# Kernel optimization log

Measured on AMD Instinct MI355X. Metric: run time of the kernel, lower is better.

The kernel has to match this reference:

```python
import jax, jax.numpy as jnp
import numpy as np

EPS = 1e-12  # matches torch F.normalize default eps


def _l2norm(x):
    n = jnp.linalg.norm(x, axis=-1, keepdims=True)
    return x / jnp.maximum(n, EPS)


def setup_inputs() -> dict:
    key = jax.random.key(0)
    k1, k2, k3, k4 = jax.random.split(key, 4)
    B, N, Lq, Ld, D = 64, 16, 32, 256, 128
    query_rep = jax.random.normal(k1, (B, Lq, D), jnp.float32)
    doc_reps = jax.random.normal(k2, (B, N, Ld, D), jnp.float32)
    doc_mask = jax.random.randint(k3, (B, N, Ld), 0, 2).astype(jnp.int32)
    labels = jax.random.normal(k4, (B, 2 * N), jnp.float32)
    return {"query_rep": query_rep, "doc_reps": doc_reps,
            "doc_mask": doc_mask, "labels": labels}


def reference(query_rep, doc_reps, doc_mask, labels):
    # ColBERT MaxSim: normalize query tokens (no mask, as in original),
    # mask+normalize doc tokens, bmm, max over doc tokens, sum over query tokens.
    q = _l2norm(query_rep)                                   # [B,Lq,D]
    d = _l2norm(doc_reps * doc_mask[..., None].astype(doc_reps.dtype))  # [B,N,Ld,D]
    tok = jnp.einsum('bqd,bnld->bnql', q, d)                 # [B,N,Lq,Ld]
    scores = tok.max(axis=-1).sum(axis=-1)                   # [B,N]

    # Pairwise ranking loss
    N = scores.shape[1]
    ys = labels[:, :N]
    idx = labels[:, N:]
    diffs = jnp.triu(scores[:, :, None] - scores[:, None, :])    # [B,N,N], lower tri zeroed
    weights = jnp.abs(idx[:, :, None] - idx[:, None, :])
    pairs = (ys[:, :, None] - ys[:, None, :]) > 0
    losses = jnp.log1p(jnp.exp(-diffs)) * weights
    return jnp.sum(jnp.where(pairs, losses, 0.0))
```

## Files before the change

### kernel.cpp

```cpp
#include <hip/hip_runtime.h>
#include <cmath>

#define EPSN 1e-12f

typedef _Float16 half8 __attribute__((ext_vector_type(8)));
typedef float f32x4 __attribute__((ext_vector_type(4)));

__global__ __launch_bounds__(256, 4) void scores_kernel(
    const float* __restrict__ qr, const float* __restrict__ doc,
    const int* __restrict__ mask, float* __restrict__ pmax) {
    __shared__ __align__(16) char Aimg[16384];
    __shared__ __align__(16) char Bimg[16384];
    __shared__ float ssPart[256];
    __shared__ float invS[128];
    __shared__ float wq[4][32];

    int t = threadIdx.x, g = blockIdx.x;
    int bn = g >> 1, h = g & 1, b = g >> 5;
    int w = t >> 6, lane = t & 63, col = lane & 15;
    int tok = t & 127, kh = t >> 7;

    const float4* dsrc = (const float4*)(doc + ((size_t)bn * 256 + h * 128 + tok) * 128) + kh * 4;
    float4 rA0 = dsrc[0], rA1 = dsrc[1], rA2 = dsrc[2], rA3 = dsrc[3];
    float4 rB0, rB1, rB2, rB3;
    int mymask = 0;
    if (t < 128) mymask = mask[bn * 256 + h * 128 + t];

    {
        int row = t >> 3, jb = t & 7;
        const float4* qsrc = (const float4*)(qr + ((size_t)b * 32 + row) * 128 + jb * 16);
        float4 v[4];
#pragma unroll
        for (int i = 0; i < 4; ++i) v[i] = qsrc[i];
        float ss = 0.f;
#pragma unroll
        for (int i = 0; i < 4; ++i)
            ss += v[i].x*v[i].x + v[i].y*v[i].y + v[i].z*v[i].z + v[i].w*v[i].w;
        ss += __shfl_xor(ss, 1); ss += __shfl_xor(ss, 2); ss += __shfl_xor(ss, 4);
        float inv = 1.0f / fmaxf(sqrtf(ss), EPSN);
        int qt = row >> 4, kstep = jb >> 1;
#pragma unroll
        for (int khh = 0; khh < 2; ++khh) {
            float xs[8] = { v[2*khh].x,   v[2*khh].y,   v[2*khh].z,   v[2*khh].w,
                            v[2*khh+1].x, v[2*khh+1].y, v[2*khh+1].z, v[2*khh+1].w };
            half8 hh, hl;
#pragma unroll
            for (int e = 0; e < 8; ++e) {
                float x = xs[e] * inv;
                _Float16 hv = (_Float16)x;
                hh[e] = hv;
                hl[e] = (_Float16)(x - (float)hv);
            }
            int quad = (jb & 1) * 2 + khh;
            int base = ((qt * 4 + kstep) * 2) * 1024 + ((row & 15) + quad * 16) * 16;
            *(half8*)(Aimg + base)        = hh;
            *(half8*)(Aimg + base + 1024) = hl;
        }
    }
    asm volatile("s_waitcnt lgkmcnt(0)" ::: "memory");
    __builtin_amdgcn_s_barrier();

    f32x4 acc[2][2];
    f32x4 zero = {0.f, 0.f, 0.f, 0.f};
    acc[0][0] = zero; acc[0][1] = zero; acc[1][0] = zero; acc[1][1] = zero;
    float ss_d = 0.f;

    int tile8 = tok >> 4;
    int bo_base = tile8 * 2048 + (2 * kh) * 256 + (tok & 15) * 16;

#define CHUNK(C, P0, P1, P2, P3, N0, N1, N2, N3, ISLAST) do {                 \
    if (!(ISLAST)) {                                                          \
        N0 = dsrc[(C + 1) * 8 + 0]; N1 = dsrc[(C + 1) * 8 + 1];               \
        N2 = dsrc[(C + 1) * 8 + 2]; N3 = dsrc[(C + 1) * 8 + 3];               \
    }                                                                         \
    ss_d += P0.x*P0.x + P0.y*P0.y + P0.z*P0.z + P0.w*P0.w;                    \
    ss_d += P1.x*P1.x + P1.y*P1.y + P1.z*P1.z + P1.w*P1.w;                    \
    ss_d += P2.x*P2.x + P2.y*P2.y + P2.z*P2.z + P2.w*P2.w;                    \
    ss_d += P3.x*P3.x + P3.y*P3.y + P3.z*P3.z + P3.w*P3.w;                    \
    {                                                                         \
        float xa[8] = { P0.x, P0.y, P0.z, P0.w, P1.x, P1.y, P1.z, P1.w };     \
        float xb[8] = { P2.x, P2.y, P2.z, P2.w, P3.x, P3.y, P3.z, P3.w };     \
        half8 hha, hla, hhb, hlb;                                             \
        _Pragma("unroll")                                                     \
        for (int e = 0; e < 8; ++e) {                                         \
            float x = xa[e]; _Float16 hv = (_Float16)x;                       \
            hha[e] = hv; hla[e] = (_Float16)(x - (float)hv);                  \
            float y = xb[e]; _Float16 hw = (_Float16)y;                       \
            hhb[e] = hw; hlb[e] = (_Float16)(y - (float)hw);                  \
        }                                                                     \
        *(half8*)(Bimg + bo_base)              = hha;                         \
        *(half8*)(Bimg + bo_base + 1024)       = hla;                         \
        *(half8*)(Bimg + bo_base + 256)        = hhb;                         \
        *(half8*)(Bimg + bo_base + 256 + 1024) = hlb;                         \
    }                                                                         \
    if (ISLAST) ssPart[t] = ss_d;                                             \
    asm volatile("s_waitcnt lgkmcnt(0)" ::: "memory");                        \
    __builtin_amdgcn_s_barrier();                                             \
    if ((ISLAST) && t < 128) {                                                \
        float sst = ssPart[t] + ssPart[t + 128];                              \
        invS[t] = mymask ? (1.0f / fmaxf(sqrtf(sst), EPSN)) : 0.0f;           \
    }                                                                         \
    {                                                                         \
        int lo = lane << 4;                                                   \
        half8 a0h = *(const half8*)(Aimg + (((C) * 2 + 0) << 10) + lo);       \
        half8 a0l = *(const half8*)(Aimg + (((C) * 2 + 1) << 10) + lo);       \
        half8 a1h = *(const half8*)(Aimg + (((4 + (C)) * 2 + 0) << 10) + lo); \
        half8 a1l = *(const half8*)(Aimg + (((4 + (C)) * 2 + 1) << 10) + lo); \
        _Pragma("unroll")                                                     \
        for (int nt = 0; nt < 2; ++nt) {                                      \
            int tile = w * 2 + nt;                                            \
            half8 bh = *(const half8*)(Bimg + tile * 2048 + lo);              \
            half8 bl = *(const half8*)(Bimg + tile * 2048 + 1024 + lo);       \
            acc[0][nt] = __builtin_amdgcn_mfma_f32_16x16x32_f16(a0l, bh, acc[0][nt], 0, 0, 0); \
            acc[0][nt] = __builtin_amdgcn_mfma_f32_16x16x32_f16(a0h, bl, acc[0][nt], 0, 0, 0); \
            acc[0][nt] = __builtin_amdgcn_mfma_f32_16x16x32_f16(a0h, bh, acc[0][nt], 0, 0, 0); \
            acc[1][nt] = __builtin_amdgcn_mfma_f32_16x16x32_f16(a1l, bh, acc[1][nt], 0, 0, 0); \
            acc[1][nt] = __builtin_amdgcn_mfma_f32_16x16x32_f16(a1h, bl, acc[1][nt], 0, 0, 0); \
            acc[1][nt] = __builtin_amdgcn_mfma_f32_16x16x32_f16(a1h, bh, acc[1][nt], 0, 0, 0); \
        }                                                                     \
    }                                                                         \
    asm volatile("s_waitcnt lgkmcnt(0)" ::: "memory");                        \
    __builtin_amdgcn_s_barrier();                                             \
} while (0)

    CHUNK(0, rA0, rA1, rA2, rA3, rB0, rB1, rB2, rB3, false);
    CHUNK(1, rB0, rB1, rB2, rB3, rA0, rA1, rA2, rA3, false);
    CHUNK(2, rA0, rA1, rA2, rA3, rB0, rB1, rB2, rB3, false);
    CHUNK(3, rB0, rB1, rB2, rB3, rA0, rA1, rA2, rA3, true);
#undef CHUNK

    float inv0 = invS[w * 32 + col];
    float inv1 = invS[w * 32 + 16 + col];
    float m8[8];
#pragma unroll
    for (int qt = 0; qt < 2; ++qt)
#pragma unroll
        for (int rr = 0; rr < 4; ++rr)
            m8[qt * 4 + rr] = fmaxf(acc[qt][0][rr] * inv0, acc[qt][1][rr] * inv1);
#pragma unroll
    for (int off = 1; off < 16; off <<= 1)
#pragma unroll
        for (int i = 0; i < 8; ++i) m8[i] = fmaxf(m8[i], __shfl_xor(m8[i], off));
    if (col == 0) {
        int rg = lane >> 4;
#pragma unroll
        for (int qt = 0; qt < 2; ++qt)
#pragma unroll
            for (int rr = 0; rr < 4; ++rr) wq[w][qt * 16 + rg * 4 + rr] = m8[qt * 4 + rr];
    }
    __syncthreads();
    if (w == 0 && lane < 32) {
        float v = fmaxf(fmaxf(wq[0][lane], wq[1][lane]), fmaxf(wq[2][lane], wq[3][lane]));
        pmax[(size_t)g * 32 + lane] = v;
    }
}

__global__ __launch_bounds__(256) void lossb_kernel(const float* __restrict__ pmax,
                                                    const float* __restrict__ labels,
                                                    float* __restrict__ partial) {
    __shared__ float pmL[1024];
    __shared__ float sc[16], ysS[16], idxS[16];
    __shared__ float wsum[4];
    int b = blockIdx.x, t = threadIdx.x;
    ((float4*)pmL)[t] = ((const float4*)(pmax + (size_t)b * 1024))[t];
    if (t < 16) { ysS[t] = labels[b * 32 + t]; idxS[t] = labels[b * 32 + 16 + t]; }
    __syncthreads();
    {
        int n = t >> 4, qq = t & 15;
        float v = fmaxf(pmL[n * 64 + qq],      pmL[n * 64 + 32 + qq])
                + fmaxf(pmL[n * 64 + 16 + qq], pmL[n * 64 + 48 + qq]);
        v += __shfl_xor(v, 1); v += __shfl_xor(v, 2);
        v += __shfl_xor(v, 4); v += __shfl_xor(v, 8);
        if (qq == 0) sc[n] = v;
    }
    __syncthreads();
    int i = t >> 4, j = t & 15;
    float v = 0.f;
    if (ysS[i] - ysS[j] > 0.f) {
        float wgt = fabsf(idxS[i] - idxS[j]);
        float d = (i <= j) ? (sc[i] - sc[j]) : 0.f;
        v = log1pf(expf(-d)) * wgt;
    }
#pragma unroll
    for (int off = 1; off < 64; off <<= 1) v += __shfl_xor(v, off);
    int lane = t & 63;
    if (lane == 0) wsum[t >> 6] = v;
    __syncthreads();
    if (t == 0) partial[b] = wsum[0] + wsum[1] + wsum[2] + wsum[3];
}

__global__ void lossfin_kernel(const float* __restrict__ partial, float* __restrict__ out) {
    int t = threadIdx.x;
    float v = partial[t];
#pragma unroll
    for (int off = 1; off < 64; off <<= 1) v += __shfl_xor(v, off);
    if (t == 0) out[0] = v;
}

extern "C" void kernel_launch(void* const* d_in, const int* in_sizes, int n_in,
                              void* d_out, int out_size, void* d_ws, size_t ws_size,
                              hipStream_t stream) {
    const float* qr     = (const float*)d_in[0];
    const float* doc    = (const float*)d_in[1];
    const int*   dmask  = (const int*)d_in[2];
    const float* labels = (const float*)d_in[3];
    float* out = (float*)d_out;

    float* pmax    = (float*)d_ws;
    float* partial = pmax + 2048 * 32;

    scores_kernel<<<2048, 256, 0, stream>>>(qr, doc, dmask, pmax);
    lossb_kernel<<<64, 256, 0, stream>>>(pmax, labels, partial);
    lossfin_kernel<<<1, 64, 0, stream>>>(partial, out);
}
```

Before: 35.01 us.

## Coalesce doc loads, use shuffle norm reduction, and merge loss kernels

```diff
diff --git a/kernel.cpp b/kernel.cpp
--- a/kernel.cpp
+++ b/kernel.cpp
@@ -4,6 +4,7 @@
 #define EPSN 1e-12f
 
 typedef _Float16 half8 __attribute__((ext_vector_type(8)));
+typedef _Float16 half4 __attribute__((ext_vector_type(4)));
 typedef float f32x4 __attribute__((ext_vector_type(4)));
 
 __global__ __launch_bounds__(256, 4) void scores_kernel(
@@ -11,20 +12,25 @@
     const int* __restrict__ mask, float* __restrict__ pmax) {
     __shared__ __align__(16) char Aimg[16384];
     __shared__ __align__(16) char Bimg[16384];
-    __shared__ float ssPart[256];
     __shared__ float invS[128];
+    __shared__ int   maskS[128];
     __shared__ float wq[4][32];
 
     int t = threadIdx.x, g = blockIdx.x;
     int bn = g >> 1, h = g & 1, b = g >> 5;
     int w = t >> 6, lane = t & 63, col = lane & 15;
-    int tok = t & 127, kh = t >> 7;
-
-    const float4* dsrc = (const float4*)(doc + ((size_t)bn * 256 + h * 128 + tok) * 128) + kh * 4;
-    float4 rA0 = dsrc[0], rA1 = dsrc[1], rA2 = dsrc[2], rA3 = dsrc[3];
+
+    int u  = t >> 3;
+    int kq = t & 7;
+
+    const float4* dbase = (const float4*)(doc + ((size_t)bn * 256 + h * 128) * 128);
+    int fi0 = u * 32 + kq;
+
+    float4 rA0 = dbase[fi0 + 0], rA1 = dbase[fi0 + 1024];
+    float4 rA2 = dbase[fi0 + 2048], rA3 = dbase[fi0 + 3072];
     float4 rB0, rB1, rB2, rB3;
-    int mymask = 0;
-    if (t < 128) mymask = mask[bn * 256 + h * 128 + t];
+
+    if (t < 128) maskS[t] = mask[bn * 256 + h * 128 + t];
 
     {
         int row = t >> 3, jb = t & 7;
@@ -63,42 +69,53 @@
     f32x4 acc[2][2];
     f32x4 zero = {0.f, 0.f, 0.f, 0.f};
     acc[0][0] = zero; acc[0][1] = zero; acc[1][0] = zero; acc[1][1] = zero;
-    float ss_d = 0.f;
-
-    int tile8 = tok >> 4;
-    int bo_base = tile8 * 2048 + (2 * kh) * 256 + (tok & 15) * 16;
+    float ss0 = 0.f, ss1 = 0.f, ss2 = 0.f, ss3 = 0.f;
+
+    int bwbase = (u >> 4) * 2048 + (((kq >> 1) * 16 + (u & 15)) << 4) + (kq & 1) * 8;
+
+#define CVT4(P, HH, HL) do {                                                  \
+    float xs_[4] = { P.x, P.y, P.z, P.w };                                    \
+    _Pragma("unroll")                                                         \
+    for (int e_ = 0; e_ < 4; ++e_) {                                          \
+        float x_ = xs_[e_]; _Float16 hv_ = (_Float16)x_;                      \
+        HH[e_] = hv_; HL[e_] = (_Float16)(x_ - (float)hv_);                   \
+    }                                                                         \
+} while (0)
 
 #define CHUNK(C, P0, P1, P2, P3, N0, N1, N2, N3, ISLAST) do {                 \
     if (!(ISLAST)) {                                                          \
-        N0 = dsrc[(C + 1) * 8 + 0]; N1 = dsrc[(C + 1) * 8 + 1];               \
-        N2 = dsrc[(C + 1) * 8 + 2]; N3 = dsrc[(C + 1) * 8 + 3];               \
-    }                                                                         \
-    ss_d += P0.x*P0.x + P0.y*P0.y + P0.z*P0.z + P0.w*P0.w;                    \
-    ss_d += P1.x*P1.x + P1.y*P1.y + P1.z*P1.z + P1.w*P1.w;                    \
-    ss_d += P2.x*P2.x + P2.y*P2.y + P2.z*P2.z + P2.w*P2.w;                    \
-    ss_d += P3.x*P3.x + P3.y*P3.y + P3.z*P3.z + P3.w*P3.w;                    \
+        N0 = dbase[fi0 + (C + 1) * 8];        N1 = dbase[fi0 + 1024 + (C + 1) * 8]; \
+        N2 = dbase[fi0 + 2048 + (C + 1) * 8]; N3 = dbase[fi0 + 3072 + (C + 1) * 8]; \
+    }                                                                         \
+    ss0 += P0.x*P0.x + P0.y*P0.y + P0.z*P0.z + P0.w*P0.w;                     \
+    ss1 += P1.x*P1.x + P1.y*P1.y + P1.z*P1.z + P1.w*P1.w;                     \
+    ss2 += P2.x*P2.x + P2.y*P2.y + P2.z*P2.z + P2.w*P2.w;                     \
+    ss3 += P3.x*P3.x + P3.y*P3.y + P3.z*P3.z + P3.w*P3.w;                     \
     {                                                                         \
-        float xa[8] = { P0.x, P0.y, P0.z, P0.w, P1.x, P1.y, P1.z, P1.w };     \
-        float xb[8] = { P2.x, P2.y, P2.z, P2.w, P3.x, P3.y, P3.z, P3.w };     \
-        half8 hha, hla, hhb, hlb;                                             \
-        _Pragma("unroll")                                                     \
-        for (int e = 0; e < 8; ++e) {                                         \
-            float x = xa[e]; _Float16 hv = (_Float16)x;                       \
-            hha[e] = hv; hla[e] = (_Float16)(x - (float)hv);                  \
-            float y = xb[e]; _Float16 hw = (_Float16)y;                       \
-            hhb[e] = hw; hlb[e] = (_Float16)(y - (float)hw);                  \
-        }                                                                     \
-        *(half8*)(Bimg + bo_base)              = hha;                         \
-        *(half8*)(Bimg + bo_base + 1024)       = hla;                         \
-        *(half8*)(Bimg + bo_base + 256)        = hhb;                         \
-        *(half8*)(Bimg + bo_base + 256 + 1024) = hlb;                         \
-    }                                                                         \
-    if (ISLAST) ssPart[t] = ss_d;                                             \
+        half4 h0, l0, h1, l1, h2, l2, h3, l3;                                 \
+        CVT4(P0, h0, l0); CVT4(P1, h1, l1); CVT4(P2, h2, l2); CVT4(P3, h3, l3); \
+        *(half4*)(Bimg + bwbase + 0)            = h0;                         \
+        *(half4*)(Bimg + bwbase + 1024)         = l0;                         \
+        *(half4*)(Bimg + bwbase + 4096)         = h1;                         \
+        *(half4*)(Bimg + bwbase + 4096 + 1024)  = l1;                         \
+        *(half4*)(Bimg + bwbase + 8192)         = h2;                         \
+        *(half4*)(Bimg + bwbase + 8192 + 1024)  = l2;                         \
+        *(half4*)(Bimg + bwbase + 12288)        = h3;                         \
+        *(half4*)(Bimg + bwbase + 12288 + 1024) = l3;                         \
+    }                                                                         \
     asm volatile("s_waitcnt lgkmcnt(0)" ::: "memory");                        \
     __builtin_amdgcn_s_barrier();                                             \
-    if ((ISLAST) && t < 128) {                                                \
-        float sst = ssPart[t] + ssPart[t + 128];                              \
-        invS[t] = mymask ? (1.0f / fmaxf(sqrtf(sst), EPSN)) : 0.0f;           \
+    if (ISLAST) {                                                             \
+        ss0 += __shfl_xor(ss0, 1); ss0 += __shfl_xor(ss0, 2); ss0 += __shfl_xor(ss0, 4); \
+        ss1 += __shfl_xor(ss1, 1); ss1 += __shfl_xor(ss1, 2); ss1 += __shfl_xor(ss1, 4); \
+        ss2 += __shfl_xor(ss2, 1); ss2 += __shfl_xor(ss2, 2); ss2 += __shfl_xor(ss2, 4); \
+        ss3 += __shfl_xor(ss3, 1); ss3 += __shfl_xor(ss3, 2); ss3 += __shfl_xor(ss3, 4); \
+        if (kq == 0) {                                                        \
+            invS[u]      = maskS[u]      ? (1.0f / fmaxf(sqrtf(ss0), EPSN)) : 0.0f; \
+            invS[u + 32] = maskS[u + 32] ? (1.0f / fmaxf(sqrtf(ss1), EPSN)) : 0.0f; \
+            invS[u + 64] = maskS[u + 64] ? (1.0f / fmaxf(sqrtf(ss2), EPSN)) : 0.0f; \
+            invS[u + 96] = maskS[u + 96] ? (1.0f / fmaxf(sqrtf(ss3), EPSN)) : 0.0f; \
+        }                                                                     \
     }                                                                         \
     {                                                                         \
         int lo = lane << 4;                                                   \
@@ -128,6 +145,7 @@
     CHUNK(2, rA0, rA1, rA2, rA3, rB0, rB1, rB2, rB3, false);
     CHUNK(3, rB0, rB1, rB2, rB3, rA0, rA1, rA2, rA3, true);
 #undef CHUNK
+#undef CVT4
 
     float inv0 = invS[w * 32 + col];
     float inv1 = invS[w * 32 + 16 + col];
@@ -155,46 +173,50 @@
     }
 }
 
-__global__ __launch_bounds__(256) void lossb_kernel(const float* __restrict__ pmax,
+__global__ __launch_bounds__(1024) void loss_kernel(const float* __restrict__ pmax,
                                                     const float* __restrict__ labels,
-                                                    float* __restrict__ partial) {
-    __shared__ float pmL[1024];
-    __shared__ float sc[16], ysS[16], idxS[16];
-    __shared__ float wsum[4];
-    int b = blockIdx.x, t = threadIdx.x;
-    ((float4*)pmL)[t] = ((const float4*)(pmax + (size_t)b * 1024))[t];
-    if (t < 16) { ysS[t] = labels[b * 32 + t]; idxS[t] = labels[b * 32 + 16 + t]; }
+                                                    float* __restrict__ out) {
+    __shared__ float scL[1024];
+    __shared__ float labL[2048];
+    __shared__ float wsum[16];
+    int t = threadIdx.x;
+    labL[t] = labels[t];
+    labL[t + 1024] = labels[t + 1024];
+    {
+        const float4* p0 = (const float4*)(pmax + (size_t)t * 64);
+        float s = 0.f;
+#pragma unroll
+        for (int i = 0; i < 8; ++i) {
+            float4 a = p0[i];
+            float4 bq = p0[i + 8];
+            s += fmaxf(a.x, bq.x) + fmaxf(a.y, bq.y) + fmaxf(a.z, bq.z) + fmaxf(a.w, bq.w);
+        }
+        scL[t] = s;
+    }
     __syncthreads();
-    {
-        int n = t >> 4, qq = t & 15;
-        float v = fmaxf(pmL[n * 64 + qq],      pmL[n * 64 + 32 + qq])
-                + fmaxf(pmL[n * 64 + 16 + qq], pmL[n * 64 + 48 + qq]);
-        v += __shfl_xor(v, 1); v += __shfl_xor(v, 2);
-        v += __shfl_xor(v, 4); v += __shfl_xor(v, 8);
-        if (qq == 0) sc[n] = v;
-    }
+    float total = 0.f;
+#pragma unroll
+    for (int it = 0; it < 16; ++it) {
+        int p = t + it * 1024;
+        int b = p >> 8, ij = p & 255, i = ij >> 4, j = ij & 15;
+        float ysi = labL[b * 32 + i], ysj = labL[b * 32 + j];
+        if (ysi - ysj > 0.f) {
+            float wgt = fabsf(labL[b * 32 + 16 + i] - labL[b * 32 + 16 + j]);
+            float d = (i <= j) ? (scL[b * 16 + i] - scL[b * 16 + j]) : 0.f;
+            total += log1pf(expf(-d)) * wgt;
+        }
+    }
+#pragma unroll
+    for (int off = 1; off < 64; off <<= 1) total += __shfl_xor(total, off);
+    int lane = t & 63;
+    if (lane == 0) wsum[t >> 6] = total;
     __syncthreads();
-    int i = t >> 4, j = t & 15;
-    float v = 0.f;
-    if (ysS[i] - ysS[j] > 0.f) {
-        float wgt = fabsf(idxS[i] - idxS[j]);
-        float d = (i <= j) ? (sc[i] - sc[j]) : 0.f;
-        v = log1pf(expf(-d)) * wgt;
-    }
-#pragma unroll
-    for (int off = 1; off < 64; off <<= 1) v += __shfl_xor(v, off);
-    int lane = t & 63;
-    if (lane == 0) wsum[t >> 6] = v;
-    __syncthreads();
-    if (t == 0) partial[b] = wsum[0] + wsum[1] + wsum[2] + wsum[3];
-}
-
-__global__ void lossfin_kernel(const float* __restrict__ partial, float* __restrict__ out) {
-    int t = threadIdx.x;
-    float v = partial[t];
-#pragma unroll
-    for (int off = 1; off < 64; off <<= 1) v += __shfl_xor(v, off);
-    if (t == 0) out[0] = v;
+    if (t < 64) {
+        float v = (t < 16) ? wsum[t] : 0.f;
+#pragma unroll
+        for (int off = 1; off < 64; off <<= 1) v += __shfl_xor(v, off);
+        if (t == 0) out[0] = v;
+    }
 }
 
 extern "C" void kernel_launch(void* const* d_in, const int* in_sizes, int n_in,
@@ -206,10 +228,8 @@
     const float* labels = (const float*)d_in[3];
     float* out = (float*)d_out;
 
-    float* pmax    = (float*)d_ws;
-    float* partial = pmax + 2048 * 32;
+    float* pmax = (float*)d_ws;
 
     scores_kernel<<<2048, 256, 0, stream>>>(qr, doc, dmask, pmax);
-    lossb_kernel<<<64, 256, 0, stream>>>(pmax, labels, partial);
-    lossfin_kernel<<<1, 64, 0, stream>>>(partial, out);
+    loss_kernel<<<1, 1024, 0, stream>>>(pmax, labels, out);
 }
```

New measurement: 55.91 us. 59.7% more time.

## Process full document per block and merge loss into single kernel

Applied to the files above, without the earlier changes.

```diff
diff --git a/kernel.cpp b/kernel.cpp
--- a/kernel.cpp
+++ b/kernel.cpp
@@ -8,23 +8,23 @@
 
 __global__ __launch_bounds__(256, 4) void scores_kernel(
     const float* __restrict__ qr, const float* __restrict__ doc,
-    const int* __restrict__ mask, float* __restrict__ pmax) {
+    const int* __restrict__ mask, float* __restrict__ scores) {
     __shared__ __align__(16) char Aimg[16384];
     __shared__ __align__(16) char Bimg[16384];
     __shared__ float ssPart[256];
     __shared__ float invS[128];
+    __shared__ int   maskS[256];
     __shared__ float wq[4][32];
 
     int t = threadIdx.x, g = blockIdx.x;
-    int bn = g >> 1, h = g & 1, b = g >> 5;
+    int b = g >> 4;
     int w = t >> 6, lane = t & 63, col = lane & 15;
     int tok = t & 127, kh = t >> 7;
 
-    const float4* dsrc = (const float4*)(doc + ((size_t)bn * 256 + h * 128 + tok) * 128) + kh * 4;
+    const float4* dsrc = (const float4*)(doc + ((size_t)g * 256 + tok) * 128) + kh * 4;
     float4 rA0 = dsrc[0], rA1 = dsrc[1], rA2 = dsrc[2], rA3 = dsrc[3];
     float4 rB0, rB1, rB2, rB3;
-    int mymask = 0;
-    if (t < 128) mymask = mask[bn * 256 + h * 128 + t];
+    maskS[t] = mask[g * 256 + t];
 
     {
         int row = t >> 3, jb = t & 7;
@@ -68,10 +68,10 @@
     int tile8 = tok >> 4;
     int bo_base = tile8 * 2048 + (2 * kh) * 256 + (tok & 15) * 16;
 
-#define CHUNK(C, P0, P1, P2, P3, N0, N1, N2, N3, ISLAST) do {                 \
-    if (!(ISLAST)) {                                                          \
-        N0 = dsrc[(C + 1) * 8 + 0]; N1 = dsrc[(C + 1) * 8 + 1];               \
-        N2 = dsrc[(C + 1) * 8 + 2]; N3 = dsrc[(C + 1) * 8 + 3];               \
+#define CHUNK(H, C, P0, P1, P2, P3, N0, N1, N2, N3, PREF, NEXTOFF, LASTC) do { \
+    if (PREF) {                                                               \
+        N0 = dsrc[(NEXTOFF) + 0]; N1 = dsrc[(NEXTOFF) + 1];                   \
+        N2 = dsrc[(NEXTOFF) + 2]; N3 = dsrc[(NEXTOFF) + 3];                   \
     }                                                                         \
     ss_d += P0.x*P0.x + P0.y*P0.y + P0.z*P0.z + P0.w*P0.w;                    \
     ss_d += P1.x*P1.x + P1.y*P1.y + P1.z*P1.z + P1.w*P1.w;                    \
@@ -93,12 +93,12 @@
         *(half8*)(Bimg + bo_base + 256)        = hhb;                         \
         *(half8*)(Bimg + bo_base + 256 + 1024) = hlb;                         \
     }                                                                         \
-    if (ISLAST) ssPart[t] = ss_d;                                             \
+    if (LASTC) { ssPart[t] = ss_d; ss_d = 0.f; }                              \
     asm volatile("s_waitcnt lgkmcnt(0)" ::: "memory");                        \
     __builtin_amdgcn_s_barrier();                                             \
-    if ((ISLAST) && t < 128) {                                                \
+    if ((LASTC) && t < 128) {                                                 \
         float sst = ssPart[t] + ssPart[t + 128];                              \
-        invS[t] = mymask ? (1.0f / fmaxf(sqrtf(sst), EPSN)) : 0.0f;           \
+        invS[t] = maskS[((H) << 7) | t] ? (1.0f / fmaxf(sqrtf(sst), EPSN)) : 0.0f; \
     }                                                                         \
     {                                                                         \
         int lo = lane << 4;                                                   \
@@ -123,78 +123,92 @@
     __builtin_amdgcn_s_barrier();                                             \
 } while (0)
 
-    CHUNK(0, rA0, rA1, rA2, rA3, rB0, rB1, rB2, rB3, false);
-    CHUNK(1, rB0, rB1, rB2, rB3, rA0, rA1, rA2, rA3, false);
-    CHUNK(2, rA0, rA1, rA2, rA3, rB0, rB1, rB2, rB3, false);
-    CHUNK(3, rB0, rB1, rB2, rB3, rA0, rA1, rA2, rA3, true);
+#define EPI_TILE(FIRST) do {                                                  \
+    float inv0 = invS[w * 32 + col];                                          \
+    float inv1 = invS[w * 32 + 16 + col];                                     \
+    float m8[8];                                                              \
+    _Pragma("unroll")                                                         \
+    for (int qt = 0; qt < 2; ++qt)                                            \
+        _Pragma("unroll")                                                     \
+        for (int rr = 0; rr < 4; ++rr)                                        \
+            m8[qt * 4 + rr] = fmaxf(acc[qt][0][rr] * inv0, acc[qt][1][rr] * inv1); \
+    _Pragma("unroll")                                                         \
+    for (int off = 1; off < 16; off <<= 1)                                    \
+        _Pragma("unroll")                                                     \
+        for (int i = 0; i < 8; ++i) m8[i] = fmaxf(m8[i], __shfl_xor(m8[i], off)); \
+    if (col == 0) {                                                           \
+        int rg = lane >> 4;           \
+        _Pragma("unroll")                                                     \
+        for (int qt = 0; qt < 2; ++qt)                                        \
+            _Pragma("unroll")                                                 \
+            for (int rr = 0; rr < 4; ++rr) {                                  \
+                int idx = qt * 16 + rg * 4 + rr;                              \
+                wq[w][idx] = (FIRST) ? m8[qt * 4 + rr]                        \
+                                     : fmaxf(wq[w][idx], m8[qt * 4 + rr]);    \
+            }                                                                 \
+    }                                                                         \
+} while (0)
+
+    CHUNK(0, 0, rA0, rA1, rA2, rA3, rB0, rB1, rB2, rB3, 1, 8,    0);
+    CHUNK(0, 1, rB0, rB1, rB2, rB3, rA0, rA1, rA2, rA3, 1, 16,   0);
+    CHUNK(0, 2, rA0, rA1, rA2, rA3, rB0, rB1, rB2, rB3, 1, 24,   0);
+    CHUNK(0, 3, rB0, rB1, rB2, rB3, rA0, rA1, rA2, rA3, 1, 4096, 1);
+    EPI_TILE(true);
+    acc[0][0] = zero; acc[0][1] = zero; acc[1][0] = zero; acc[1][1] = zero;
+    CHUNK(1, 0, rA0, rA1, rA2, rA3, rB0, rB1, rB2, rB3, 1, 4104, 0);
+    CHUNK(1, 1, rB0, rB1, rB2, rB3, rA0, rA1, rA2, rA3, 1, 4112, 0);
+    CHUNK(1, 2, rA0, rA1, rA2, rA3, rB0, rB1, rB2, rB3, 1, 4120, 0);
+    CHUNK(1, 3, rB0, rB1, rB2, rB3, rA0, rA1, rA2, rA3, 0, 0,    1);
+    EPI_TILE(false);
 #undef CHUNK
-
-    float inv0 = invS[w * 32 + col];
-    float inv1 = invS[w * 32 + 16 + col];
-    float m8[8];
-#pragma unroll
-    for (int qt = 0; qt < 2; ++qt)
-#pragma unroll
-        for (int rr = 0; rr < 4; ++rr)
-            m8[qt * 4 + rr] = fmaxf(acc[qt][0][rr] * inv0, acc[qt][1][rr] * inv1);
-#pragma unroll
-    for (int off = 1; off < 16; off <<= 1)
-#pragma unroll
-        for (int i = 0; i < 8; ++i) m8[i] = fmaxf(m8[i], __shfl_xor(m8[i], off));
-    if (col == 0) {
-        int rg = lane >> 4;
-#pragma unroll
-        for (int qt = 0; qt < 2; ++qt)
-#pragma unroll
-            for (int rr = 0; rr < 4; ++rr) wq[w][qt * 16 + rg * 4 + rr] = m8[qt * 4 + rr];
-    }
+#undef EPI_TILE
+
+    asm volatile("s_waitcnt lgkmcnt(0)" ::: "memory");
+    __builtin_amdgcn_s_barrier();
+    if (w == 0) {
+        float v = 0.f;
+        if (lane < 32)
+            v = fmaxf(fmaxf(wq[0][lane], wq[1][lane]), fmaxf(wq[2][lane], wq[3][lane]));
+#pragma unroll
+        for (int off = 1; off < 64; off <<= 1) v += __shfl_xor(v, off);
+        if (lane == 0) scores[g] = v;
+    }
+}
+
+__global__ __launch_bounds__(1024) void loss_kernel(const float* __restrict__ scores,
+                                                    const float* __restrict__ labels,
+                                                    float* __restrict__ out) {
+    __shared__ float scL[1024];
+    __shared__ float labL[2048];
+    __shared__ float wsum[16];
+    int t = threadIdx.x;
+    labL[t] = labels[t];
+    labL[t + 1024] = labels[t + 1024];
+    scL[t] = scores[t];
     __syncthreads();
-    if (w == 0 && lane < 32) {
-        float v = fmaxf(fmaxf(wq[0][lane], wq[1][lane]), fmaxf(wq[2][lane], wq[3][lane]));
-        pmax[(size_t)g * 32 + lane] = v;
-    }
-}
-
-__global__ __launch_bounds__(256) void lossb_kernel(const float* __restrict__ pmax,
-                                                    const float* __restrict__ labels,
-                                                    float* __restrict__ partial) {
-    __shared__ float pmL[1024];
-    __shared__ float sc[16], ysS[16], idxS[16];
-    __shared__ float wsum[4];
-    int b = blockIdx.x, t = threadIdx.x;
-    ((float4*)pmL)[t] = ((const float4*)(pmax + (size_t)b * 1024))[t];
-    if (t < 16) { ysS[t] = labels[b * 32 + t]; idxS[t] = labels[b * 32 + 16 + t]; }
+    float total = 0.f;
+#pragma unroll
+    for (int it = 0; it < 16; ++it) {
+        int p = t + it * 1024;
+        int b = p >> 8, ij = p & 255, i = ij >> 4, j = ij & 15;
+        float ysi = labL[b * 32 + i], ysj = labL[b * 32 + j];
+        if (ysi - ysj > 0.f) {
+            float wgt = fabsf(labL[b * 32 + 16 + i] - labL[b * 32 + 16 + j]);
+            float d = (i <= j) ? (scL[b * 16 + i] - scL[b * 16 + j]) : 0.f;
+            total += log1pf(expf(-d)) * wgt;
+        }
+    }
+#pragma unroll
+    for (int off = 1; off < 64; off <<= 1) total += __shfl_xor(total, off);
+    int lane = t & 63;
+    if (lane == 0) wsum[t >> 6] = total;
     __syncthreads();
-    {
-        int n = t >> 4, qq = t & 15;
-        float v = fmaxf(pmL[n * 64 + qq],      pmL[n * 64 + 32 + qq])
-                + fmaxf(pmL[n * 64 + 16 + qq], pmL[n * 64 + 48 + qq]);
-        v += __shfl_xor(v, 1); v += __shfl_xor(v, 2);
-        v += __shfl_xor(v, 4); v += __shfl_xor(v, 8);
-        if (qq == 0) sc[n] = v;
-    }
-    __syncthreads();
-    int i = t >> 4, j = t & 15;
-    float v = 0.f;
-    if (ysS[i] - ysS[j] > 0.f) {
-        float wgt = fabsf(idxS[i] - idxS[j]);
-        float d = (i <= j) ? (sc[i] - sc[j]) : 0.f;
-        v = log1pf(expf(-d)) * wgt;
-    }
-#pragma unroll
-    for (int off = 1; off < 64; off <<= 1) v += __shfl_xor(v, off);
-    int lane = t & 63;
-    if (lane == 0) wsum[t >> 6] = v;
-    __syncthreads();
-    if (t == 0) partial[b] = wsum[0] + wsum[1] + wsum[2] + wsum[3];
-}
-
-__global__ void lossfin_kernel(const float* __restrict__ partial, float* __restrict__ out) {
-    int t = threadIdx.x;
-    float v = partial[t];
-#pragma unroll
-    for (int off = 1; off < 64; off <<= 1) v += __shfl_xor(v, off);
-    if (t == 0) out[0] = v;
+    if (t < 64) {
+        float v = (t < 16) ? wsum[t] : 0.f;
+#pragma unroll
+        for (int off = 1; off < 64; off <<= 1) v += __shfl_xor(v, off);
+        if (t == 0) out[0] = v;
+    }
 }
 
 extern "C" void kernel_launch(void* const* d_in, const int* in_sizes, int n_in,
@@ -206,10 +220,8 @@
     const float* labels = (const float*)d_in[3];
     float* out = (float*)d_out;
 
-    float* pmax    = (float*)d_ws;
-    float* partial = pmax + 2048 * 32;
-
-    scores_kernel<<<2048, 256, 0, stream>>>(qr, doc, dmask, pmax);
-    lossb_kernel<<<64, 256, 0, stream>>>(pmax, labels, partial);
-    lossfin_kernel<<<1, 64, 0, stream>>>(partial, out);
+    float* scores = (float*)d_ws;
+
+    scores_kernel<<<1024, 256, 0, stream>>>(qr, doc, dmask, scores);
+    loss_kernel<<<1, 1024, 0, stream>>>(scores, labels, out);
 }
```

Measured after the change: 45.89 us. +31.1%, slower.
